# Kernel tuning notes

Hardware: AMD Instinct MI355X
Metric: run time of the kernel (lower is better)

Reference implementation:

```python
import jax, jax.numpy as jnp
import numpy as np

SIGMA_LIKELIHOOD = 0.1  # hardcoded in the original forward
LOG_SQRT_2PI = 0.5 * float(np.log(2.0 * np.pi))


def _expected_mu(pred):
    """Vectorized calculateExpectedValues over the batch.
    pred: [B, 7] in molecule order O2, N2, H2, CO2, H2O, CH4, NH3.
    Returns mu: [B, 7] expected abundance per molecule (0 for unclassified).
    """
    O2, N2, H2, CO2, H2O, CH4, NH3 = (pred[:, i] for i in range(7))
    H = 2 * H2 + 2 * H2O + 3 * NH3 + 4 * CH4
    C = CO2 + CH4
    O = 2 * O2 + 2 * CO2 + H2O
    N = 2 * N2 + NH3

    condA = H > 2 * O + 4 * C
    mA1 = condA & (3 * N < H - 2 * O - 4 * C)
    mA2 = condA & ~mA1
    mB = ~condA & (2 * O > H + 4 * C)
    mC = ~condA & ~mB & (jnp.abs(H + C + O + N - 1.0) < 1e-3)

    def sd(num, den, m):  # masked safe divide (avoids NaN in unselected branches)
        return jnp.where(m, num / jnp.where(m, den, 1.0), 0.0)

    z = jnp.zeros_like(H)
    # branch A1: D = H - N - 2C
    dA1 = H - N - 2 * C
    muA1 = jnp.stack([z, z, sd(H - 2 * O - 4 * C - 3 * N, dA1, mA1), z,
                      sd(2 * O, dA1, mA1), sd(2 * C, dA1, mA1), sd(2 * N, dA1, mA1)], axis=-1)
    # branch A2: D = H + 2C + 3N + 4O
    dA2 = H + 2 * C + 3 * N + 4 * O
    muA2 = jnp.stack([z, sd(3 * N + 4 * C + 2 * O - H, dA2, mA2), z, z,
                      sd(6 * O, dA2, mA2), sd(6 * C, dA2, mA2), sd(2 * H - 8 * C - 4 * O, dA2, mA2)], axis=-1)
    # branch B: D = H + 2O + 2N
    dB = H + 2 * O + 2 * N
    muB = jnp.stack([sd(2 * O - H - 4 * C, dB, mB), sd(2 * N, dB, mB), z,
                     sd(4 * C, dB, mB), sd(2 * H, dB, mB), z, z], axis=-1)
    # branch C: D1 = H + 2O + 2N, D2 = 2H + 4O + 4N
    d1 = H + 2 * O + 2 * N
    d2 = 2 * H + 4 * O + 4 * N
    muC = jnp.stack([z, sd(2 * N, d1, mC), z, sd(2 * O + 4 * C - H, d2, mC),
                     sd(H + 2 * O - 4 * C, d1, mC), sd(H - 2 * O + 4 * C, d2, mC), z], axis=-1)
    # masks are mutually exclusive -> sum selects the right branch (unknown -> 0)
    return muA1 + muA2 + muB + muC


def setup_inputs() -> dict:
    key = jax.random.key(0)
    k1, k2, k3, k4 = jax.random.split(key, 4)
    B, S = 8192, 4096
    predAbun = jax.random.uniform(k1, (B, 7), dtype=jnp.float32)
    sigmaPrior = jax.random.uniform(k2, (B, 7), dtype=jnp.float32) * 0.5 + 0.1
    yReal = jax.random.normal(k3, (B, S), dtype=jnp.float32)
    ySim = jax.random.normal(k4, (B, S), dtype=jnp.float32)
    return {"predAbun": predAbun, "sigmaPrior": sigmaPrior, "yReal": yReal, "ySim": ySim}


def reference(predAbun, sigmaPrior, yReal, ySim):
    # prior: batched vectorization of the per-sample Python loop in calculatePrior
    mu = _expected_mu(predAbun)                                  # [B, 7]
    per_elem = (LOG_SQRT_2PI + jnp.log(sigmaPrior)
                + (predAbun - mu) ** 2 / (2.0 * sigmaPrior ** 2))  # [B, 7]
    prior = jnp.sum(per_elem) / predAbun.shape[0]                # scalar (mean over batch of per-sample sums)
    # likelihood: per-sample gaussian NLL of spectra
    mse = jnp.mean((yReal - ySim) ** 2, axis=1)                  # [B]
    likelihood = mse / (2.0 * SIGMA_LIKELIHOOD ** 2)             # [B]
    posterior = likelihood + prior                               # [B]
    return posterior
```

## Files before the change

### kernel.cpp

```cpp
#include <hip/hip_runtime.h>
#include <math.h>

#define LOG_SQRT_2PI 0.9189385332046727f

typedef float f32x4 __attribute__((ext_vector_type(4)));

__global__ __launch_bounds__(256) void prior_partials(
        const float* __restrict__ pred,
        const float* __restrict__ sigma,
        float* __restrict__ ws, int B, int pb) {
    float s = 0.0f;
    for (int b = blockIdx.x * 256 + threadIdx.x; b < B; b += pb * 256) {
        const float* p  = pred  + (size_t)b * 7;
        const float* sg = sigma + (size_t)b * 7;
        float O2 = p[0], N2 = p[1], H2 = p[2], CO2 = p[3];
        float H2O = p[4], CH4 = p[5], NH3 = p[6];

        float H = 2.f*H2 + 2.f*H2O + 3.f*NH3 + 4.f*CH4;
        float C = CO2 + CH4;
        float O = 2.f*O2 + 2.f*CO2 + H2O;
        float N = 2.f*N2 + NH3;

        float mu0=0.f, mu1=0.f, mu2=0.f, mu3=0.f, mu4=0.f, mu5=0.f, mu6=0.f;

        bool condA = (H > 2.f*O + 4.f*C);
        if (condA) {
            if (3.f*N < H - 2.f*O - 4.f*C) {
                float D = H - N - 2.f*C;
                mu2 = (H - 2.f*O - 4.f*C - 3.f*N) / D;
                mu4 = (2.f*O) / D;
                mu5 = (2.f*C) / D;
                mu6 = (2.f*N) / D;
            } else {
                float D = H + 2.f*C + 3.f*N + 4.f*O;
                mu1 = (3.f*N + 4.f*C + 2.f*O - H) / D;
                mu4 = (6.f*O) / D;
                mu5 = (6.f*C) / D;
                mu6 = (2.f*H - 8.f*C - 4.f*O) / D;
            }
        } else if (2.f*O > H + 4.f*C) {
            float D = H + 2.f*O + 2.f*N;
            mu0 = (2.f*O - H - 4.f*C) / D;
            mu1 = (2.f*N) / D;
            mu3 = (4.f*C) / D;
            mu4 = (2.f*H) / D;
        } else if (fabsf(H + C + O + N - 1.0f) < 1e-3f) {
            float D1 = H + 2.f*O + 2.f*N;
            float D2 = 2.f*H + 4.f*O + 4.f*N;
            mu1 = (2.f*N) / D1;
            mu3 = (2.f*O + 4.f*C - H) / D2;
            mu4 = (H + 2.f*O - 4.f*C) / D1;
            mu5 = (H - 2.f*O + 4.f*C) / D2;
        }

        float mu[7] = {mu0, mu1, mu2, mu3, mu4, mu5, mu6};
        #pragma unroll
        for (int i = 0; i < 7; ++i) {
            float d = p[i] - mu[i];
            float sgi = sg[i];
            s += LOG_SQRT_2PI + logf(sgi) + d * d / (2.0f * sgi * sgi);
        }
    }

    #pragma unroll
    for (int off = 32; off > 0; off >>= 1) s += __shfl_down(s, off, 64);
    __shared__ float wsum[4];
    int lane = threadIdx.x & 63, w = threadIdx.x >> 6;
    if (lane == 0) wsum[w] = s;
    __syncthreads();
    if (threadIdx.x == 0) ws[blockIdx.x] = wsum[0] + wsum[1] + wsum[2] + wsum[3];
}

template <int NITER>
__global__ __launch_bounds__(256) void loss_kernel_t(
        const float* __restrict__ yReal,
        const float* __restrict__ ySim,
        const float* __restrict__ partials,
        float* __restrict__ out, int S, float c_mse, float c_prior, int pb) {
    int b = blockIdx.x;
    const f32x4* yr = (const f32x4*)(yReal + (size_t)b * S);
    const f32x4* ys = (const f32x4*)(ySim  + (size_t)b * S);

    float u = (threadIdx.x < pb) ? partials[threadIdx.x] * c_prior : 0.0f;

    float s = 0.0f;
    #pragma unroll
    for (int k = 0; k < NITER; ++k) {
        int i = threadIdx.x + k * 256;
        f32x4 a = __builtin_nontemporal_load(yr + i);
        f32x4 c = ys[i];
        float d0 = a.x - c.x, d1 = a.y - c.y;
        float d2 = a.z - c.z, d3 = a.w - c.w;
        s += d0*d0 + d1*d1 + d2*d2 + d3*d3;
    }
    u += s * c_mse;

    #pragma unroll
    for (int off = 32; off > 0; off >>= 1) u += __shfl_down(u, off, 64);
    __shared__ float wsum[4];
    int lane = threadIdx.x & 63, w = threadIdx.x >> 6;
    if (lane == 0) wsum[w] = u;
    __syncthreads();
    if (threadIdx.x == 0) out[b] = wsum[0] + wsum[1] + wsum[2] + wsum[3];
}

__global__ __launch_bounds__(256) void loss_kernel_g(
        const float* __restrict__ yReal,
        const float* __restrict__ ySim,
        const float* __restrict__ partials,
        float* __restrict__ out, int S, float c_mse, float c_prior, int pb) {
    int b = blockIdx.x;
    const float* yr = yReal + (size_t)b * S;
    const float* ys = ySim  + (size_t)b * S;

    float u = (threadIdx.x < pb) ? partials[threadIdx.x] * c_prior : 0.0f;

    float s = 0.0f;
    int n4 = S >> 2;
    const f32x4* yr4 = (const f32x4*)yr;
    const f32x4* ys4 = (const f32x4*)ys;
    for (int i = threadIdx.x; i < n4; i += 256) {
        f32x4 a = __builtin_nontemporal_load(yr4 + i);
        f32x4 c = ys4[i];
        float d0 = a.x - c.x, d1 = a.y - c.y;
        float d2 = a.z - c.z, d3 = a.w - c.w;
        s += d0*d0 + d1*d1 + d2*d2 + d3*d3;
    }
    for (int i = (n4 << 2) + threadIdx.x; i < S; i += 256) {
        float d = yr[i] - ys[i];
        s += d * d;
    }
    u += s * c_mse;

    #pragma unroll
    for (int off = 32; off > 0; off >>= 1) u += __shfl_down(u, off, 64);
    __shared__ float wsum[4];
    int lane = threadIdx.x & 63, w = threadIdx.x >> 6;
    if (lane == 0) wsum[w] = u;
    __syncthreads();
    if (threadIdx.x == 0) out[b] = wsum[0] + wsum[1] + wsum[2] + wsum[3];
}

extern "C" void kernel_launch(void* const* d_in, const int* in_sizes, int n_in,
                              void* d_out, int out_size, void* d_ws, size_t ws_size,
                              hipStream_t stream) {
    const float* pred  = (const float*)d_in[0];
    const float* sigma = (const float*)d_in[1];
    const float* yReal = (const float*)d_in[2];
    const float* ySim  = (const float*)d_in[3];
    float* out = (float*)d_out;
    float* ws  = (float*)d_ws;

    int B = in_sizes[0] / 7;
    int S = in_sizes[2] / B;

    int pb = (B + 255) / 256;
    if (pb > 256) pb = 256;

    prior_partials<<<pb, 256, 0, stream>>>(pred, sigma, ws, B, pb);

    float c_mse   = 50.0f / (float)S;
    float c_prior = 1.0f / (float)B;

    if ((S & 3) == 0 && (S >> 2) == 1024) {
        loss_kernel_t<4><<<B, 256, 0, stream>>>(yReal, ySim, ws, out, S, c_mse, c_prior, pb);
    } else if ((S & 3) == 0 && (S >> 2) == 2048) {
        loss_kernel_t<8><<<B, 256, 0, stream>>>(yReal, ySim, ws, out, S, c_mse, c_prior, pb);
    } else {
        loss_kernel_g<<<B, 256, 0, stream>>>(yReal, ySim, ws, out, S, c_mse, c_prior, pb);
    }
}
```

Before: 48.01 us.

## Fuse prior and MSE into one persistent cooperative kernel with grid sync

Replaces the two-kernel launch (prior partials, then per-row loss) with one persistent cooperative kernel sized to occupancy. Each block computes a strided slice of prior partials, then loops over its rows computing per-row MSE held in shared memory. A grid-wide sync follows, after which every block sums all prior partials and writes its rows. This removes the second launch and the launch-to-launch dependency, and lets the prior work overlap with streaming. It also drops the nontemporal load hint, and adds host-side occupancy queries on every call plus the cost of the grid barrier.

```diff
diff --git a/kernel.cpp b/kernel.cpp
--- a/kernel.cpp
+++ b/kernel.cpp
@@ -1,67 +1,130 @@
 #include <hip/hip_runtime.h>
+#include <hip/hip_cooperative_groups.h>
 #include <math.h>
 
+namespace cg = cooperative_groups;
+
 #define LOG_SQRT_2PI 0.9189385332046727f
-
 typedef float f32x4 __attribute__((ext_vector_type(4)));
+
+__device__ __forceinline__ float prior_row(const float* __restrict__ pred,
+                                           const float* __restrict__ sigma,
+                                           int b) {
+    const float* p  = pred  + (size_t)b * 7;
+    const float* sg = sigma + (size_t)b * 7;
+    float O2 = p[0], N2 = p[1], H2 = p[2], CO2 = p[3];
+    float H2O = p[4], CH4 = p[5], NH3 = p[6];
+
+    float H = 2.f*H2 + 2.f*H2O + 3.f*NH3 + 4.f*CH4;
+    float C = CO2 + CH4;
+    float O = 2.f*O2 + 2.f*CO2 + H2O;
+    float N = 2.f*N2 + NH3;
+
+    float mu0=0.f, mu1=0.f, mu2=0.f, mu3=0.f, mu4=0.f, mu5=0.f, mu6=0.f;
+
+    bool condA = (H > 2.f*O + 4.f*C);
+    if (condA) {
+        if (3.f*N < H - 2.f*O - 4.f*C) {
+            float D = H - N - 2.f*C;
+            mu2 = (H - 2.f*O - 4.f*C - 3.f*N) / D;
+            mu4 = (2.f*O) / D;
+            mu5 = (2.f*C) / D;
+            mu6 = (2.f*N) / D;
+        } else {
+            float D = H + 2.f*C + 3.f*N + 4.f*O;
+            mu1 = (3.f*N + 4.f*C + 2.f*O - H) / D;
+            mu4 = (6.f*O) / D;
+            mu5 = (6.f*C) / D;
+            mu6 = (2.f*H - 8.f*C - 4.f*O) / D;
+        }
+    } else if (2.f*O > H + 4.f*C) {
+        float D = H + 2.f*O + 2.f*N;
+        mu0 = (2.f*O - H - 4.f*C) / D;
+        mu1 = (2.f*N) / D;
+        mu3 = (4.f*C) / D;
+        mu4 = (2.f*H) / D;
+    } else if (fabsf(H + C + O + N - 1.0f) < 1e-3f) {
+        float D1 = H + 2.f*O + 2.f*N;
+        float D2 = 2.f*H + 4.f*O + 4.f*N;
+        mu1 = (2.f*N) / D1;
+        mu3 = (2.f*O + 4.f*C - H) / D2;
+        mu4 = (H + 2.f*O - 4.f*C) / D1;
+        mu5 = (H - 2.f*O + 4.f*C) / D2;
+    }
+
+    float mu[7] = {mu0, mu1, mu2, mu3, mu4, mu5, mu6};
+    float s = 0.f;
+    #pragma unroll
+    for (int i = 0; i < 7; ++i) {
+        float d = p[i] - mu[i];
+        float sgi = sg[i];
+        s += LOG_SQRT_2PI + logf(sgi) + d * d / (2.0f * sgi * sgi);
+    }
+    return s;
+}
+
+template <int NITER>
+__global__ __launch_bounds__(256, 8) void fused_loss(
+        const float* __restrict__ pred, const float* __restrict__ sigma,
+        const float* __restrict__ yReal, const float* __restrict__ ySim,
+        float* __restrict__ ws, float* __restrict__ out,
+        int B, int S, float c_mse, float c_prior, int nb) {
+    int blk  = blockIdx.x;
+    int lane = threadIdx.x & 63, w = threadIdx.x >> 6;
+
+    float ps = 0.f;
+    for (int b = blk + nb * threadIdx.x; b < B; b += nb * 256)
+        ps += prior_row(pred, sigma, b);
+    #pragma unroll
+    for (int off = 32; off; off >>= 1) ps += __shfl_down(ps, off, 64);
+    __shared__ float psh[4];
+    if (lane == 0) psh[w] = ps;
+    __syncthreads();
+    if (threadIdx.x == 0) ws[blk] = psh[0] + psh[1] + psh[2] + psh[3];
+
+    __shared__ float wsum[4][32];
+    int nr = 0;
+    for (int row = blk; row < B; row += nb, ++nr) {
+        const f32x4* yr = (const f32x4*)(yReal + (size_t)row * S);
+        const f32x4* ys = (const f32x4*)(ySim  + (size_t)row * S);
+        float s = 0.f;
+        #pragma unroll
+        for (int k = 0; k < NITER; ++k) {
+            int i = threadIdx.x + k * 256;
+            f32x4 a = yr[i], c = ys[i];
+            f32x4 d = a - c;
+            s += d.x*d.x + d.y*d.y + d.z*d.z + d.w*d.w;
+        }
+        #pragma unroll
+        for (int off = 32; off; off >>= 1) s += __shfl_down(s, off, 64);
+        if (lane == 0) wsum[w][nr] = s;
+    }
+
+    cg::this_grid().sync();
+
+    float u = 0.f;
+    for (int i = threadIdx.x; i < nb; i += 256) u += ws[i];
+    #pragma unroll
+    for (int off = 32; off; off >>= 1) u += __shfl_down(u, off, 64);
+    __shared__ float usum[4];
+    if (lane == 0) usum[w] = u;
+    __syncthreads();
+    float total = (usum[0] + usum[1] + usum[2] + usum[3]) * c_prior;
+
+    if (threadIdx.x < nr) {
+        float ms = wsum[0][threadIdx.x] + wsum[1][threadIdx.x]
+                 + wsum[2][threadIdx.x] + wsum[3][threadIdx.x];
+        out[blk + nb * threadIdx.x] = ms * c_mse + total;
+    }
+}
 
 __global__ __launch_bounds__(256) void prior_partials(
         const float* __restrict__ pred,
         const float* __restrict__ sigma,
         float* __restrict__ ws, int B, int pb) {
     float s = 0.0f;
-    for (int b = blockIdx.x * 256 + threadIdx.x; b < B; b += pb * 256) {
-        const float* p  = pred  + (size_t)b * 7;
-        const float* sg = sigma + (size_t)b * 7;
-        float O2 = p[0], N2 = p[1], H2 = p[2], CO2 = p[3];
-        float H2O = p[4], CH4 = p[5], NH3 = p[6];
-
-        float H = 2.f*H2 + 2.f*H2O + 3.f*NH3 + 4.f*CH4;
-        float C = CO2 + CH4;
-        float O = 2.f*O2 + 2.f*CO2 + H2O;
-        float N = 2.f*N2 + NH3;
-
-        float mu0=0.f, mu1=0.f, mu2=0.f, mu3=0.f, mu4=0.f, mu5=0.f, mu6=0.f;
-
-        bool condA = (H > 2.f*O + 4.f*C);
-        if (condA) {
-            if (3.f*N < H - 2.f*O - 4.f*C) {
-                float D = H - N - 2.f*C;
-                mu2 = (H - 2.f*O - 4.f*C - 3.f*N) / D;
-                mu4 = (2.f*O) / D;
-                mu5 = (2.f*C) / D;
-                mu6 = (2.f*N) / D;
-            } else {
-                float D = H + 2.f*C + 3.f*N + 4.f*O;
-                mu1 = (3.f*N + 4.f*C + 2.f*O - H) / D;
-                mu4 = (6.f*O) / D;
-                mu5 = (6.f*C) / D;
-                mu6 = (2.f*H - 8.f*C - 4.f*O) / D;
-            }
-        } else if (2.f*O > H + 4.f*C) {
-            float D = H + 2.f*O + 2.f*N;
-            mu0 = (2.f*O - H - 4.f*C) / D;
-            mu1 = (2.f*N) / D;
-            mu3 = (4.f*C) / D;
-            mu4 = (2.f*H) / D;
-        } else if (fabsf(H + C + O + N - 1.0f) < 1e-3f) {
-            float D1 = H + 2.f*O + 2.f*N;
-            float D2 = 2.f*H + 4.f*O + 4.f*N;
-            mu1 = (2.f*N) / D1;
-            mu3 = (2.f*O + 4.f*C - H) / D2;
-            mu4 = (H + 2.f*O - 4.f*C) / D1;
-            mu5 = (H - 2.f*O + 4.f*C) / D2;
-        }
-
-        float mu[7] = {mu0, mu1, mu2, mu3, mu4, mu5, mu6};
-        #pragma unroll
-        for (int i = 0; i < 7; ++i) {
-            float d = p[i] - mu[i];
-            float sgi = sg[i];
-            s += LOG_SQRT_2PI + logf(sgi) + d * d / (2.0f * sgi * sgi);
-        }
-    }
-
+    for (int b = blockIdx.x * 256 + threadIdx.x; b < B; b += pb * 256)
+        s += prior_row(pred, sigma, b);
     #pragma unroll
     for (int off = 32; off > 0; off >>= 1) s += __shfl_down(s, off, 64);
     __shared__ float wsum[4];
@@ -69,39 +132,6 @@
     if (lane == 0) wsum[w] = s;
     __syncthreads();
     if (threadIdx.x == 0) ws[blockIdx.x] = wsum[0] + wsum[1] + wsum[2] + wsum[3];
-}
-
-template <int NITER>
-__global__ __launch_bounds__(256) void loss_kernel_t(
-        const float* __restrict__ yReal,
-        const float* __restrict__ ySim,
-        const float* __restrict__ partials,
-        float* __restrict__ out, int S, float c_mse, float c_prior, int pb) {
-    int b = blockIdx.x;
-    const f32x4* yr = (const f32x4*)(yReal + (size_t)b * S);
-    const f32x4* ys = (const f32x4*)(ySim  + (size_t)b * S);
-
-    float u = (threadIdx.x < pb) ? partials[threadIdx.x] * c_prior : 0.0f;
-
-    float s = 0.0f;
-    #pragma unroll
-    for (int k = 0; k < NITER; ++k) {
-        int i = threadIdx.x + k * 256;
-        f32x4 a = __builtin_nontemporal_load(yr + i);
-        f32x4 c = ys[i];
-        float d0 = a.x - c.x, d1 = a.y - c.y;
-        float d2 = a.z - c.z, d3 = a.w - c.w;
-        s += d0*d0 + d1*d1 + d2*d2 + d3*d3;
-    }
-    u += s * c_mse;
-
-    #pragma unroll
-    for (int off = 32; off > 0; off >>= 1) u += __shfl_down(u, off, 64);
-    __shared__ float wsum[4];
-    int lane = threadIdx.x & 63, w = threadIdx.x >> 6;
-    if (lane == 0) wsum[w] = u;
-    __syncthreads();
-    if (threadIdx.x == 0) out[b] = wsum[0] + wsum[1] + wsum[2] + wsum[3];
 }
 
 __global__ __launch_bounds__(256) void loss_kernel_g(
@@ -120,11 +150,10 @@
     const f32x4* yr4 = (const f32x4*)yr;
     const f32x4* ys4 = (const f32x4*)ys;
     for (int i = threadIdx.x; i < n4; i += 256) {
-        f32x4 a = __builtin_nontemporal_load(yr4 + i);
+        f32x4 a = yr4[i];
         f32x4 c = ys4[i];
-        float d0 = a.x - c.x, d1 = a.y - c.y;
-        float d2 = a.z - c.z, d3 = a.w - c.w;
-        s += d0*d0 + d1*d1 + d2*d2 + d3*d3;
+        f32x4 d = a - c;
+        s += d.x*d.x + d.y*d.y + d.z*d.z + d.w*d.w;
     }
     for (int i = (n4 << 2) + threadIdx.x; i < S; i += 256) {
         float d = yr[i] - ys[i];
@@ -139,6 +168,16 @@
     if (lane == 0) wsum[w] = u;
     __syncthreads();
     if (threadIdx.x == 0) out[b] = wsum[0] + wsum[1] + wsum[2] + wsum[3];
+}
+
+static void launch_fallback(const float* pred, const float* sigma,
+                            const float* yReal, const float* ySim,
+                            float* ws, float* out, int B, int S,
+                            float c_mse, float c_prior, hipStream_t stream) {
+    int pb = (B + 255) / 256;
+    if (pb > 256) pb = 256;
+    prior_partials<<<pb, 256, 0, stream>>>(pred, sigma, ws, B, pb);
+    loss_kernel_g<<<B, 256, 0, stream>>>(yReal, ySim, ws, out, S, c_mse, c_prior, pb);
 }
 
 extern "C" void kernel_launch(void* const* d_in, const int* in_sizes, int n_in,
@@ -154,19 +193,37 @@
     int B = in_sizes[0] / 7;
     int S = in_sizes[2] / B;
 
-    int pb = (B + 255) / 256;
-    if (pb > 256) pb = 256;
-
-    prior_partials<<<pb, 256, 0, stream>>>(pred, sigma, ws, B, pb);
-
     float c_mse   = 50.0f / (float)S;
     float c_prior = 1.0f / (float)B;
 
-    if ((S & 3) == 0 && (S >> 2) == 1024) {
-        loss_kernel_t<4><<<B, 256, 0, stream>>>(yReal, ySim, ws, out, S, c_mse, c_prior, pb);
-    } else if ((S & 3) == 0 && (S >> 2) == 2048) {
-        loss_kernel_t<8><<<B, 256, 0, stream>>>(yReal, ySim, ws, out, S, c_mse, c_prior, pb);
-    } else {
-        loss_kernel_g<<<B, 256, 0, stream>>>(yReal, ySim, ws, out, S, c_mse, c_prior, pb);
-    }
-}
+    if (S == 4096 || S == 2048) {
+        int dev = 0;
+        hipGetDevice(&dev);
+        int numCU = 0;
+        hipDeviceGetAttribute(&numCU, hipDeviceAttributeMultiprocessorCount, dev);
+        int occ = 0;
+        if (S == 4096)
+            hipOccupancyMaxActiveBlocksPerMultiprocessor(&occ, fused_loss<4>, 256, 0);
+        else
+            hipOccupancyMaxActiveBlocksPerMultiprocessor(&occ, fused_loss<2>, 256, 0);
+        long nb_l = (long)occ * (long)numCU;
+        if (nb_l > B) nb_l = B;
+        int nb = (int)nb_l;
+
+        if (nb > 0 && (B + nb - 1) / nb <= 32) {
+            void* args[] = {(void*)&pred, (void*)&sigma, (void*)&yReal, (void*)&ySim,
+                            (void*)&ws, (void*)&out, (void*)&B, (void*)&S,
+                            (void*)&c_mse, (void*)&c_prior, (void*)&nb};
+            hipError_t e;
+            if (S == 4096)
+                e = hipLaunchCooperativeKernel(fused_loss<4>, dim3(nb), dim3(256),
+                                               args, 0, stream);
+            else
+                e = hipLaunchCooperativeKernel(fused_loss<2>, dim3(nb), dim3(256),
+                                               args, 0, stream);
+            if (e == hipSuccess) return;
+        }
+    }
+
+    launch_fallback(pred, sigma, yReal, ySim, ws, out, B, S, c_mse, c_prior, stream);
+}
```

After: 174.7 us. 264% more time.
